# Kernel optimization log

Measured on AMD Instinct MI355X. Metric: run time of the kernel, lower is better.

Reference implementation:

```python
import jax, jax.numpy as jnp
import numpy as np

B, C, H, W = 16, 512, 32, 32
KC = C // 8  # key_channels = 64


def setup_inputs() -> dict:
    key = jax.random.key(0)
    ks = jax.random.split(key, 6)
    s_in = 1.0 / np.sqrt(C)
    return {
        "x": jax.random.normal(ks[0], (B, C, H, W), dtype=jnp.float32),
        "Wq": jax.random.normal(ks[1], (KC, C), dtype=jnp.float32) * s_in,
        "bq": jnp.zeros((KC,), dtype=jnp.float32),
        "Wk": jax.random.normal(ks[2], (KC, C), dtype=jnp.float32) * s_in,
        "bk": jnp.zeros((KC,), dtype=jnp.float32),
        "Wv": jax.random.normal(ks[3], (C, C), dtype=jnp.float32) * s_in,
        "bv": jnp.zeros((C,), dtype=jnp.float32),
        "Wo": jax.random.normal(ks[4], (C, C), dtype=jnp.float32) * s_in,
        "bo": jnp.zeros((C,), dtype=jnp.float32),
        "gamma": jnp.zeros((1,), dtype=jnp.float32),
    }


def reference(x, Wq, bq, Wk, bk, Wv, bv, Wo, bo, gamma):
    b, c, h, w = x.shape
    n = h * w
    kc = Wq.shape[0]
    xf = x.reshape(b, c, n)  # [B, C, N]
    # 1x1 convs == channel matmuls
    q = jnp.einsum('kc,bcn->bnk', Wq, xf) + bq  # [B, N, KC]
    k = jnp.einsum('kc,bcn->bkn', Wk, xf) + bk[None, :, None]  # [B, KC, N]
    v = jnp.einsum('vc,bcn->bnv', Wv, xf) + bv  # [B, N, C]
    scale = jnp.asarray(kc, x.dtype) ** -0.5
    att = jax.nn.softmax(jnp.einsum('bnk,bkm->bnm', q, k) * scale, axis=-1)  # [B, N, N]
    out = jnp.einsum('bnm,bmv->bnv', att, v)  # [B, N, C]
    out = jnp.einsum('cv,bnv->bcn', Wo, out) + bo[None, :, None]  # [B, C, N]
    out = gamma[0] * out + xf
    return out.reshape(b, c, h, w)
```

## Files before the change

### kernel.cpp

```cpp
#include <hip/hip_runtime.h>
#include <cstddef>


typedef unsigned short ushort_t;
typedef __attribute__((ext_vector_type(8))) short bf16x8;
typedef __attribute__((ext_vector_type(4))) float f32x4;
typedef __attribute__((ext_vector_type(2))) float f32x2;
typedef __attribute__((ext_vector_type(2))) unsigned u32x2;

#define QSCALE 0.18033688011112042f

__device__ __forceinline__ ushort_t f2bf_t(float f) {
  return (ushort_t)(__float_as_uint(f) >> 16);
}
__device__ __forceinline__ unsigned pk2bf(float lo, float hi) {
  return __builtin_amdgcn_perm(__float_as_uint(hi), __float_as_uint(lo),
                               0x07060302u);
}

__device__ __forceinline__ void gload16(const ushort_t* g, ushort_t* l) {
  __builtin_amdgcn_global_load_lds(
      (const __attribute__((address_space(1))) void*)g,
      (__attribute__((address_space(3))) void*)l, 16, 0, 0);
}

template <int TM>
__device__ __forceinline__ void gemm_core(
    const ushort_t* __restrict__ A, int lda,
    const ushort_t* __restrict__ B, int ldb,
    int K, int m0, int n0,
    ushort_t* As, ushort_t* Bs, f32x4 (*acc)[4])
{
  constexpr int MT  = TM / 32;
  constexpr int WTM = TM / 2;
  const int t = threadIdx.x;
  const int lane = t & 63, quad = lane >> 4, l15 = lane & 15;
  const int w = t >> 6, wm = w >> 1, wn = w & 1;
  const int rr = (lane >> 3) & 7;
  const int gg = (lane & 7) ^ rr;

  auto stage = [&](int k0, int pbuf) {
    ushort_t* Ad = As + pbuf * (TM * 64);
    ushort_t* Bd = Bs + pbuf * (128 * 64);
    #pragma unroll
    for (int i = 0; i < TM / 32; ++i) {
      const int mrow = w * (TM / 4) + i * 8;
      gload16(A + (size_t)(m0 + mrow + rr) * lda + k0 + gg * 8, Ad + mrow * 64);
    }
    #pragma unroll
    for (int i = 0; i < 4; ++i) {
      const int mrow = w * 32 + i * 8;
      gload16(B + (size_t)(n0 + mrow + rr) * ldb + k0 + gg * 8, Bd + mrow * 64);
    }
  };

  stage(0, 0);

  #pragma unroll
  for (int i = 0; i < MT; ++i)
    #pragma unroll
    for (int j = 0; j < 4; ++j) acc[i][j] = (f32x4){0.f, 0.f, 0.f, 0.f};

  __syncthreads();

  int pb = 0;
  for (int k0 = 0; k0 < K; k0 += 64) {
    if (k0 + 64 < K) stage(k0 + 64, pb ^ 1);
    const ushort_t* Ac = As + pb * (TM * 64);
    const ushort_t* Bc = Bs + pb * (128 * 64);
    #pragma unroll
    for (int kk = 0; kk < 2; ++kk) {
      const int gq = kk * 4 + quad;
      const int sg = (gq ^ (l15 & 7)) * 8;
      bf16x8 af[MT], bfr[4];
      #pragma unroll
      for (int i = 0; i < MT; ++i)
        af[i] = *(const bf16x8*)(Ac + (wm * WTM + i * 16 + l15) * 64 + sg);
      #pragma unroll
      for (int j = 0; j < 4; ++j)
        bfr[j] = *(const bf16x8*)(Bc + (wn * 64 + j * 16 + l15) * 64 + sg);
      #pragma unroll
      for (int i = 0; i < MT; ++i)
        #pragma unroll
        for (int j = 0; j < 4; ++j)
          acc[i][j] = __builtin_amdgcn_mfma_f32_16x16x32_bf16(
              af[i], bfr[j], acc[i][j], 0, 0, 0);
    }
    __syncthreads();
    pb ^= 1;
  }
}

template <int TM, class F>
__device__ __forceinline__ void store_bf16(
    ushort_t* lds, ushort_t* __restrict__ out, int ldo, int m0, int n0,
    f32x4 (*acc)[4], F f)
{
  constexpr int MT = TM / 32, WTM = TM / 2, SI = TM / 16;
  const int t = threadIdx.x;
  const int lane = t & 63, quad = lane >> 4, l15 = lane & 15;
  const int w = t >> 6, wm = w >> 1, wn = w & 1;
  #pragma unroll
  for (int i = 0; i < MT; ++i)
    #pragma unroll
    for (int j = 0; j < 4; ++j)
      #pragma unroll
      for (int r = 0; r < 4; ++r) {
        const int rl = wm * WTM + i * 16 + quad * 4 + r;
        const int cl = wn * 64 + j * 16 + l15;
        lds[rl * 136 + cl] = f2bf_t(f(i, j, r, rl, cl, acc[i][j][r]));
      }
  __syncthreads();
  #pragma unroll
  for (int i = 0; i < SI; ++i) {
    const int s = i * 256 + t, m = s >> 4, g = s & 15;
    const uint4 v = *(const uint4*)(lds + m * 136 + g * 8);
    *(uint4*)(out + (size_t)(m0 + m) * ldo + n0 + g * 8) = v;
  }
}

__global__ __launch_bounds__(256) void prep_x(
    const float* __restrict__ x,
    const float* __restrict__ Wq, const float* __restrict__ Wk,
    const float* __restrict__ Wv, const float* __restrict__ Wo,
    ushort_t* __restrict__ xbfT, ushort_t* __restrict__ Wqk,
    ushort_t* __restrict__ Wvb, ushort_t* __restrict__ Wob)
{
  __shared__ float T[64 * 66];
  const int t = threadIdx.x;
  if (blockIdx.y == 8) {
    const int id = blockIdx.z * 16 + blockIdx.x;
    #pragma unroll
    for (int p = 0; p < 5; ++p) {
      const int s = p * 256 + t;
      if (s < 1152) {
        const int u = id * 1152 + s;
        const int e = u * 2;
        float f0, f1;
        if (e < 32768)       { f0 = Wq[e];         f1 = Wq[e + 1]; }
        else if (e < 65536)  { f0 = Wk[e - 32768]; f1 = Wk[e - 32767]; }
        else if (e < 327680) { f0 = Wv[e - 65536]; f1 = Wv[e - 65535]; }
        else                 { f0 = Wo[e - 327680]; f1 = Wo[e - 327679]; }
        const unsigned pk = pk2bf(f0, f1);
        if (e < 65536)       *((unsigned*)Wqk + u) = pk;
        else if (e < 327680) *((unsigned*)Wvb + (u - 32768)) = pk;
        else                 *((unsigned*)Wob + (u - 163840)) = pk;
      }
    }
    return;
  }
  const int b = blockIdx.z, c0 = blockIdx.y * 64, n0 = blockIdx.x * 64;
  const float* xb = x + ((size_t)b * 512 + c0) * 1024 + n0;
  const int njf = t & 15, ci0 = t >> 4;
  #pragma unroll
  for (int p = 0; p < 4; ++p) {
    const int ci = p * 16 + ci0;
    const f32x4 v = *(const f32x4*)(xb + (size_t)ci * 1024 + njf * 4);
    float* d = &T[ci * 66 + njf * 4];
    *(f32x2*)(d)     = (f32x2){v[0], v[1]};
    *(f32x2*)(d + 2) = (f32x2){v[2], v[3]};
  }
  __syncthreads();
  const int c4 = (t & 15) * 4, nr0 = t >> 4;
  #pragma unroll
  for (int p = 0; p < 4; ++p) {
    const int nr = p * 16 + nr0;
    const float a0 = T[(c4 + 0) * 66 + nr];
    const float a1 = T[(c4 + 1) * 66 + nr];
    const float a2 = T[(c4 + 2) * 66 + nr];
    const float a3 = T[(c4 + 3) * 66 + nr];
    const u32x2 pkv = {pk2bf(a0, a1), pk2bf(a2, a3)};
    *(u32x2*)&xbfT[((size_t)b * 1024 + n0 + nr) * 512 + c0 + c4] = pkv;
  }
}

__global__ __launch_bounds__(256) void k1_fused(
    const ushort_t* __restrict__ xbfT, const ushort_t* __restrict__ Wqk,
    const ushort_t* __restrict__ Wvb,
    const float* __restrict__ bq, const float* __restrict__ bk,
    const float* __restrict__ bv,
    ushort_t* __restrict__ qkt, ushort_t* __restrict__ vt2)
{
  __shared__ __align__(16) ushort_t lds[32768];
  const unsigned lin = blockIdx.x;
  const unsigned wid = (lin & 7) * 96 + (lin >> 3);
  const int b = wid / 48, r = wid % 48;
  const int t = threadIdx.x, lane = t & 63, quad = lane >> 4, l15 = lane & 15;
  const int w = t >> 6, wm = w >> 1, wn = w & 1;
  if (r < 32) {
    const int m0 = (r >> 3) * 128, n0 = (r & 7) * 128;
    f32x4 acc[4][4];
    gemm_core<128>(Wvb, 512, xbfT + (size_t)b * 524288, 512, 512, m0, n0,
                   lds, lds + 16384, acc);
    float br[4][4];
    #pragma unroll
    for (int i = 0; i < 4; ++i)
      #pragma unroll
      for (int rr2 = 0; rr2 < 4; ++rr2)
        br[i][rr2] = bv[m0 + wm * 64 + i * 16 + quad * 4 + rr2];
    store_bf16<128>(lds, vt2 + (size_t)b * 524288, 1024, m0, n0, acc,
        [&](int i, int, int rr2, int, int, float v) { return v + br[i][rr2]; });
  } else {
    const int m0 = (r - 32) * 64;
    f32x4 acc[2][4];
    gemm_core<64>(xbfT + (size_t)b * 524288, 512, Wqk, 512, 512, m0, 0,
                  lds, lds + 8192, acc);
    float bc[4], qs[4];
    #pragma unroll
    for (int j = 0; j < 4; ++j) {
      const int col = wn * 64 + j * 16 + l15;
      bc[j] = (col < 64) ? bq[col] : bk[col - 64];
      qs[j] = (col < 64) ? QSCALE : 1.0f;
    }
    store_bf16<64>(lds, qkt + (size_t)b * 131072, 128, m0, 0, acc,
        [&](int, int j, int, int, int, float v) { return (v + bc[j]) * qs[j]; });
  }
}

__global__ __launch_bounds__(256) void flash_attn(
    const ushort_t* __restrict__ qkt, const ushort_t* __restrict__ vt2,
    ushort_t* __restrict__ o1)
{
  __shared__ __align__(16) ushort_t buf[33792];
  __shared__ float lsum[64][2];
  ushort_t* Ks0 = buf;
  ushort_t* Vs0 = buf + 8192;
  ushort_t* Ps0 = buf + 24576;

  const int t = threadIdx.x;
  const int lane = t & 63, quad = lane >> 4, l15 = lane & 15;
  const int w = t >> 6, wm = w >> 1, wn = w & 1;
  const int rr = (lane >> 3) & 7, gg = (lane & 7) ^ rr;

  const unsigned lin = blockIdx.x;
  const unsigned wid = (lin & 7) * 128 + (lin >> 3);
  const int b  = wid >> 6;
  const int m0 = ((wid >> 2) & 15) * 64;
  const int c0 = (wid & 3) * 128;

  const ushort_t* qb = qkt + (size_t)b * 131072;
  const ushort_t* vb = vt2 + (size_t)b * 524288;

  #pragma unroll
  for (int i = 0; i < 2; ++i) {
    const int mrow = w * 16 + i * 8;
    gload16(qb + (size_t)(m0 + mrow + rr) * 128 + gg * 8, Ps0 + mrow * 64);
  }
  asm volatile("s_waitcnt vmcnt(0)" ::: "memory");
  __builtin_amdgcn_s_barrier();

  bf16x8 af_q[2][2];
  #pragma unroll
  for (int kk = 0; kk < 2; ++kk) {
    const int sg = ((kk * 4 + quad) ^ (l15 & 7)) * 8;
    #pragma unroll
    for (int i = 0; i < 2; ++i)
      af_q[i][kk] = *(const bf16x8*)(Ps0 + (wm * 32 + i * 16 + l15) * 64 + sg);
  }

  const ushort_t* kp = qb + (size_t)(w * 16 + rr) * 128 + 64 + gg * 8;
  const ushort_t* vp = vb + (size_t)(c0 + w * 32 + rr) * 1024 + gg * 8;

  #pragma unroll
  for (int i = 0; i < 2; ++i)
    gload16(kp + i * 1024, Ks0 + (w * 16 + i * 8) * 64);
  #pragma unroll
  for (int i = 0; i < 4; ++i)
    gload16(vp + i * 8192, Vs0 + (w * 32 + i * 8) * 64);
  asm volatile("s_waitcnt vmcnt(0) lgkmcnt(0)" ::: "memory");
  __builtin_amdgcn_s_barrier();

  f32x4 accO[2][4];
  #pragma unroll
  for (int i = 0; i < 2; ++i)
    #pragma unroll
    for (int j = 0; j < 4; ++j) accO[i][j] = (f32x4){0.f, 0.f, 0.f, 0.f};
  float rsum[2][4] = {{0.f, 0.f, 0.f, 0.f}, {0.f, 0.f, 0.f, 0.f}};

  const int psw_off = (wm * 32 + quad * 4) * 72 + wn * 32 + l15;
  const int sg0 = (quad ^ (l15 & 7)) * 8;
  const int sg1 = ((4 + quad) ^ (l15 & 7)) * 8;

  const ushort_t* kpn = kp + 8192;
  const ushort_t* vpn = vp + 64;
  int p = 0;

  #pragma unroll 1
  for (int mc = 0; mc < 1024; mc += 64) {
    ushort_t* Ksd = p ? Ks0 + 4096 : Ks0;
    ushort_t* Vsd = p ? Vs0 + 8192 : Vs0;
    ushort_t* Psd = p ? Ps0 + 4608 : Ps0;
    ushort_t* Ksn = p ? Ks0 : Ks0 + 4096;
    ushort_t* Vsn = p ? Vs0 : Vs0 + 8192;

    if (mc < 960) {
      #pragma unroll
      for (int i = 0; i < 2; ++i)
        gload16(kpn + i * 1024, Ksn + (w * 16 + i * 8) * 64);
      #pragma unroll
      for (int i = 0; i < 4; ++i)
        gload16(vpn + i * 8192, Vsn + (w * 32 + i * 8) * 64);
    }

    f32x4 accS[2][2];
    #pragma unroll
    for (int i = 0; i < 2; ++i)
      #pragma unroll
      for (int j = 0; j < 2; ++j) accS[i][j] = (f32x4){0.f, 0.f, 0.f, 0.f};
    #pragma unroll
    for (int kk = 0; kk < 2; ++kk) {
      const int sg = kk ? sg1 : sg0;
      bf16x8 bk_[2];
      #pragma unroll
      for (int j = 0; j < 2; ++j)
        bk_[j] = *(const bf16x8*)(Ksd + (wn * 32 + j * 16 + l15) * 64 + sg);
      #pragma unroll
      for (int i = 0; i < 2; ++i)
        #pragma unroll
        for (int j = 0; j < 2; ++j)
          accS[i][j] = __builtin_amdgcn_mfma_f32_16x16x32_bf16(
              af_q[i][kk], bk_[j], accS[i][j], 0, 0, 0);
    }

    ushort_t* psw = Psd + psw_off;
    #pragma unroll
    for (int i = 0; i < 2; ++i)
      #pragma unroll
      for (int j = 0; j < 2; ++j)
        #pragma unroll
        for (int r2 = 0; r2 < 4; ++r2) {
          const float e = __builtin_amdgcn_exp2f(accS[i][j][r2]);
          rsum[i][r2] += e;
          psw[(i * 16 + r2) * 72 + j * 16] = f2bf_t(e);
        }

    asm volatile("s_waitcnt lgkmcnt(0)" ::: "memory");
    __builtin_amdgcn_s_barrier();

    #pragma unroll
    for (int kk = 0; kk < 2; ++kk) {
      const int gq = kk * 4 + quad;
      const int sgv = kk ? sg1 : sg0;
      bf16x8 ap[2], bv_[4];
      #pragma unroll
      for (int i = 0; i < 2; ++i)
        ap[i] = *(const bf16x8*)(Psd + (wm * 32 + i * 16 + l15) * 72 + gq * 8);
      #pragma unroll
      for (int j = 0; j < 4; ++j)
        bv_[j] = *(const bf16x8*)(Vsd + (wn * 64 + j * 16 + l15) * 64 + sgv);
      #pragma unroll
      for (int i = 0; i < 2; ++i)
        #pragma unroll
        for (int j = 0; j < 4; ++j)
          accO[i][j] = __builtin_amdgcn_mfma_f32_16x16x32_bf16(
              ap[i], bv_[j], accO[i][j], 0, 0, 0);
    }

    asm volatile("s_waitcnt vmcnt(0)" ::: "memory");
    __builtin_amdgcn_s_barrier();

    kpn += 8192;
    vpn += 64;
    p ^= 1;
  }

  #pragma unroll
  for (int i = 0; i < 2; ++i)
    #pragma unroll
    for (int r2 = 0; r2 < 4; ++r2) {
      float s = rsum[i][r2];
      #pragma unroll
      for (int d = 1; d < 16; d <<= 1) s += __shfl_xor(s, d, 16);
      if (l15 == 0) lsum[wm * 32 + i * 16 + quad * 4 + r2][wn] = s;
    }
  __syncthreads();

  ushort_t* fl_b = buf;
  #pragma unroll
  for (int i = 0; i < 2; ++i)
    #pragma unroll
    for (int r2 = 0; r2 < 4; ++r2) {
      const int row = wm * 32 + i * 16 + quad * 4 + r2;
      const float inv = 1.0f / (lsum[row][0] + lsum[row][1]);
      #pragma unroll
      for (int j = 0; j < 4; ++j)
        fl_b[row * 136 + wn * 64 + j * 16 + l15] = f2bf_t(accO[i][j][r2] * inv);
    }
  __syncthreads();
  #pragma unroll
  for (int pp = 0; pp < 4; ++pp) {
    const int s = pp * 256 + t, m = s >> 4, g = s & 15;
    const uint4 v = *(const uint4*)(fl_b + m * 136 + g * 8);
    *(uint4*)(o1 + ((size_t)b * 1024 + m0 + m) * 512 + c0 + g * 8) = v;
  }
}

__global__ __launch_bounds__(256) void k4_proj(
    const ushort_t* __restrict__ Wob, const ushort_t* __restrict__ o1,
    const float* __restrict__ bo, const float* __restrict__ gamma,
    const float* __restrict__ x, float* __restrict__ out)
{
  __shared__ __align__(16) ushort_t lds[32768];
  const unsigned lin = blockIdx.x;
  const unsigned wid = (lin & 7) * 64 + (lin >> 3);
  const int b = wid >> 5, rem = wid & 31;
  const int m0 = (rem >> 3) * 128, n0 = (rem & 7) * 128;
  f32x4 acc[4][4];
  gemm_core<128>(Wob, 512, o1 + (size_t)b * 524288, 512, 512, m0, n0,
                 lds, lds + 16384, acc);
  const int t = threadIdx.x, lane = t & 63, quad = lane >> 4, l15 = lane & 15;
  const int w = t >> 6, wm = w >> 1, wn = w & 1;
  const float g = gamma[0];
  float br[4][4];
  #pragma unroll
  for (int i = 0; i < 4; ++i)
    #pragma unroll
    for (int r2 = 0; r2 < 4; ++r2)
      br[i][r2] = bo[m0 + wm * 64 + i * 16 + quad * 4 + r2];
  float* fl = (float*)lds;
  #pragma unroll
  for (int h = 0; h < 2; ++h) {
    if (wm == h) {
      #pragma unroll
      for (int i = 0; i < 4; ++i)
        #pragma unroll
        for (int j = 0; j < 4; ++j)
          #pragma unroll
          for (int r2 = 0; r2 < 4; ++r2)
            fl[(i * 16 + quad * 4 + r2) * 132 + wn * 64 + j * 16 + l15] =
                g * (acc[i][j][r2] + br[i][r2]);
    }
    __syncthreads();
    #pragma unroll
    for (int i2 = 0; i2 < 8; ++i2) {
      const int s = i2 * 256 + t, m = s >> 5, c4 = s & 31;
      f32x4 v = *(const f32x4*)(fl + m * 132 + c4 * 4);
      const size_t gi = ((size_t)b * 512 + m0 + h * 64 + m) * 1024 + n0 + c4 * 4;
      const f32x4 xr = *(const f32x4*)(x + gi);
      v += xr;
      *(f32x4*)(out + gi) = v;
    }
    __syncthreads();
  }
}

extern "C" void kernel_launch(void* const* d_in, const int* in_sizes, int n_in,
                              void* d_out, int out_size, void* d_ws, size_t ws_size,
                              hipStream_t stream) {
  const float* x     = (const float*)d_in[0];
  const float* Wq    = (const float*)d_in[1];
  const float* bq    = (const float*)d_in[2];
  const float* Wk    = (const float*)d_in[3];
  const float* bk    = (const float*)d_in[4];
  const float* Wv    = (const float*)d_in[5];
  const float* bv    = (const float*)d_in[6];
  const float* Wo    = (const float*)d_in[7];
  const float* bo    = (const float*)d_in[8];
  const float* gamma = (const float*)d_in[9];
  float* out = (float*)d_out;

  char* wsp = (char*)d_ws;
  ushort_t* xbfT   = (ushort_t*)wsp;  wsp += (size_t)16 * 1024 * 512 * 2;
  ushort_t* Wqk_bf = (ushort_t*)wsp;  wsp += (size_t)128 * 512 * 2;
  ushort_t* Wv_bf  = (ushort_t*)wsp;  wsp += (size_t)512 * 512 * 2;
  ushort_t* Wo_bf  = (ushort_t*)wsp;  wsp += (size_t)512 * 512 * 2;
  ushort_t* qkt    = (ushort_t*)wsp;  wsp += (size_t)16 * 1024 * 128 * 2;
  ushort_t* vt2    = (ushort_t*)wsp;  wsp += (size_t)16 * 512 * 1024 * 2;
  ushort_t* o1     = xbfT;

  prep_x    <<<dim3(16, 9, 16), 256, 0, stream>>>(x, Wq, Wk, Wv, Wo,
                                                  xbfT, Wqk_bf, Wv_bf, Wo_bf);
  k1_fused  <<<768, 256, 0, stream>>>(xbfT, Wqk_bf, Wv_bf, bq, bk, bv, qkt, vt2);
  flash_attn<<<dim3(1024), 256, 0, stream>>>(qkt, vt2, o1);
  k4_proj   <<<512, 256, 0, stream>>>(Wo_bf, o1, bo, gamma, x, out);
}
```

Before: 179.0 us.

## Use 512-thread blocks with 8 waves and drop double buffering in GEMM and attention

Moves the GEMM, attention and projection kernels to 512-thread blocks of 8 waves. Each wave now computes a smaller sub-tile, and the QK GEMM tile grows to 128 rows, so fewer blocks are launched. Double-buffered LDS prefetch with hand-placed waitcnt/barrier is replaced by single-buffered load-sync-compute loops, which cuts LDS use per block. The cost is load latency no longer overlapping compute and more barriers per iteration, traded for more waves per block to hide latency.

```diff
diff --git a/kernel.cpp b/kernel.cpp
--- a/kernel.cpp
+++ b/kernel.cpp
@@ -24,96 +24,75 @@
       (__attribute__((address_space(3))) void*)l, 16, 0, 0);
 }
 
-template <int TM>
-__device__ __forceinline__ void gemm_core(
+__device__ __forceinline__ void gemm512(
     const ushort_t* __restrict__ A, int lda,
     const ushort_t* __restrict__ B, int ldb,
-    int K, int m0, int n0,
-    ushort_t* As, ushort_t* Bs, f32x4 (*acc)[4])
-{
-  constexpr int MT  = TM / 32;
-  constexpr int WTM = TM / 2;
+    int m0, int n0, ushort_t* As, ushort_t* Bs, f32x4 (*acc)[2])
+{
   const int t = threadIdx.x;
   const int lane = t & 63, quad = lane >> 4, l15 = lane & 15;
-  const int w = t >> 6, wm = w >> 1, wn = w & 1;
+  const int w = t >> 6, wm = w >> 2, wn4 = w & 3;
   const int rr = (lane >> 3) & 7;
   const int gg = (lane & 7) ^ rr;
 
-  auto stage = [&](int k0, int pbuf) {
-    ushort_t* Ad = As + pbuf * (TM * 64);
-    ushort_t* Bd = Bs + pbuf * (128 * 64);
-    #pragma unroll
-    for (int i = 0; i < TM / 32; ++i) {
-      const int mrow = w * (TM / 4) + i * 8;
-      gload16(A + (size_t)(m0 + mrow + rr) * lda + k0 + gg * 8, Ad + mrow * 64);
-    }
-    #pragma unroll
-    for (int i = 0; i < 4; ++i) {
-      const int mrow = w * 32 + i * 8;
-      gload16(B + (size_t)(n0 + mrow + rr) * ldb + k0 + gg * 8, Bd + mrow * 64);
-    }
-  };
-
-  stage(0, 0);
-
-  #pragma unroll
-  for (int i = 0; i < MT; ++i)
-    #pragma unroll
-    for (int j = 0; j < 4; ++j) acc[i][j] = (f32x4){0.f, 0.f, 0.f, 0.f};
-
-  __syncthreads();
-
-  int pb = 0;
-  for (int k0 = 0; k0 < K; k0 += 64) {
-    if (k0 + 64 < K) stage(k0 + 64, pb ^ 1);
-    const ushort_t* Ac = As + pb * (TM * 64);
-    const ushort_t* Bc = Bs + pb * (128 * 64);
+  #pragma unroll
+  for (int i = 0; i < 4; ++i)
+    #pragma unroll
+    for (int j = 0; j < 2; ++j) acc[i][j] = (f32x4){0.f, 0.f, 0.f, 0.f};
+
+  for (int k0 = 0; k0 < 512; k0 += 64) {
+    __syncthreads();
+    #pragma unroll
+    for (int i = 0; i < 2; ++i) {
+      const int mrow = w * 16 + i * 8;
+      gload16(A + (size_t)(m0 + mrow + rr) * lda + k0 + gg * 8, As + mrow * 64);
+      gload16(B + (size_t)(n0 + mrow + rr) * ldb + k0 + gg * 8, Bs + mrow * 64);
+    }
+    __syncthreads();
     #pragma unroll
     for (int kk = 0; kk < 2; ++kk) {
       const int gq = kk * 4 + quad;
       const int sg = (gq ^ (l15 & 7)) * 8;
-      bf16x8 af[MT], bfr[4];
-      #pragma unroll
-      for (int i = 0; i < MT; ++i)
-        af[i] = *(const bf16x8*)(Ac + (wm * WTM + i * 16 + l15) * 64 + sg);
-      #pragma unroll
-      for (int j = 0; j < 4; ++j)
-        bfr[j] = *(const bf16x8*)(Bc + (wn * 64 + j * 16 + l15) * 64 + sg);
-      #pragma unroll
-      for (int i = 0; i < MT; ++i)
+      bf16x8 af[4], bfr[2];
+      #pragma unroll
+      for (int i = 0; i < 4; ++i)
+        af[i] = *(const bf16x8*)(As + (wm * 64 + i * 16 + l15) * 64 + sg);
+      #pragma unroll
+      for (int j = 0; j < 2; ++j)
+        bfr[j] = *(const bf16x8*)(Bs + (wn4 * 32 + j * 16 + l15) * 64 + sg);
+      #pragma unroll
+      for (int i = 0; i < 4; ++i)
         #pragma unroll
-        for (int j = 0; j < 4; ++j)
+        for (int j = 0; j < 2; ++j)
           acc[i][j] = __builtin_amdgcn_mfma_f32_16x16x32_bf16(
               af[i], bfr[j], acc[i][j], 0, 0, 0);
     }
-    __syncthreads();
-    pb ^= 1;
-  }
-}
-
-template <int TM, class F>
-__device__ __forceinline__ void store_bf16(
+  }
+  __syncthreads();
+}
+
+template <class F>
+__device__ __forceinline__ void store_bf16_512(
     ushort_t* lds, ushort_t* __restrict__ out, int ldo, int m0, int n0,
-    f32x4 (*acc)[4], F f)
-{
-  constexpr int MT = TM / 32, WTM = TM / 2, SI = TM / 16;
+    f32x4 (*acc)[2], F f)
+{
   const int t = threadIdx.x;
   const int lane = t & 63, quad = lane >> 4, l15 = lane & 15;
-  const int w = t >> 6, wm = w >> 1, wn = w & 1;
-  #pragma unroll
-  for (int i = 0; i < MT; ++i)
-    #pragma unroll
-    for (int j = 0; j < 4; ++j)
+  const int w = t >> 6, wm = w >> 2, wn4 = w & 3;
+  #pragma unroll
+  for (int i = 0; i < 4; ++i)
+    #pragma unroll
+    for (int j = 0; j < 2; ++j)
       #pragma unroll
       for (int r = 0; r < 4; ++r) {
-        const int rl = wm * WTM + i * 16 + quad * 4 + r;
-        const int cl = wn * 64 + j * 16 + l15;
-        lds[rl * 136 + cl] = f2bf_t(f(i, j, r, rl, cl, acc[i][j][r]));
+        const int rl = wm * 64 + i * 16 + quad * 4 + r;
+        const int cl = wn4 * 32 + j * 16 + l15;
+        lds[rl * 136 + cl] = f2bf_t(f(i, j, r, acc[i][j][r]));
       }
   __syncthreads();
   #pragma unroll
-  for (int i = 0; i < SI; ++i) {
-    const int s = i * 256 + t, m = s >> 4, g = s & 15;
+  for (int i = 0; i < 4; ++i) {
+    const int s = i * 512 + t, m = s >> 4, g = s & 15;
     const uint4 v = *(const uint4*)(lds + m * 136 + g * 8);
     *(uint4*)(out + (size_t)(m0 + m) * ldo + n0 + g * 8) = v;
   }
@@ -174,101 +153,82 @@
   }
 }
 
-__global__ __launch_bounds__(256) void k1_fused(
+__global__ __launch_bounds__(512) void k1_fused(
     const ushort_t* __restrict__ xbfT, const ushort_t* __restrict__ Wqk,
     const ushort_t* __restrict__ Wvb,
     const float* __restrict__ bq, const float* __restrict__ bk,
     const float* __restrict__ bv,
     ushort_t* __restrict__ qkt, ushort_t* __restrict__ vt2)
 {
-  __shared__ __align__(16) ushort_t lds[32768];
+  __shared__ __align__(16) ushort_t lds[17408];
   const unsigned lin = blockIdx.x;
-  const unsigned wid = (lin & 7) * 96 + (lin >> 3);
-  const int b = wid / 48, r = wid % 48;
+  const unsigned wid = (lin & 7) * 80 + (lin >> 3);
+  const int b = wid / 40, r = wid % 40;
   const int t = threadIdx.x, lane = t & 63, quad = lane >> 4, l15 = lane & 15;
-  const int w = t >> 6, wm = w >> 1, wn = w & 1;
+  const int w = t >> 6, wm = w >> 2, wn4 = w & 3;
+  f32x4 acc[4][2];
   if (r < 32) {
     const int m0 = (r >> 3) * 128, n0 = (r & 7) * 128;
-    f32x4 acc[4][4];
-    gemm_core<128>(Wvb, 512, xbfT + (size_t)b * 524288, 512, 512, m0, n0,
-                   lds, lds + 16384, acc);
+    gemm512(Wvb, 512, xbfT + (size_t)b * 524288, 512, m0, n0,
+            lds, lds + 8192, acc);
     float br[4][4];
     #pragma unroll
     for (int i = 0; i < 4; ++i)
       #pragma unroll
-      for (int rr2 = 0; rr2 < 4; ++rr2)
-        br[i][rr2] = bv[m0 + wm * 64 + i * 16 + quad * 4 + rr2];
-    store_bf16<128>(lds, vt2 + (size_t)b * 524288, 1024, m0, n0, acc,
-        [&](int i, int, int rr2, int, int, float v) { return v + br[i][rr2]; });
+      for (int r2 = 0; r2 < 4; ++r2)
+        br[i][r2] = bv[m0 + wm * 64 + i * 16 + quad * 4 + r2];
+    store_bf16_512(lds, vt2 + (size_t)b * 524288, 1024, m0, n0, acc,
+        [&](int i, int, int r2, float v) { return v + br[i][r2]; });
   } else {
-    const int m0 = (r - 32) * 64;
-    f32x4 acc[2][4];
-    gemm_core<64>(xbfT + (size_t)b * 524288, 512, Wqk, 512, 512, m0, 0,
-                  lds, lds + 8192, acc);
-    float bc[4], qs[4];
-    #pragma unroll
-    for (int j = 0; j < 4; ++j) {
-      const int col = wn * 64 + j * 16 + l15;
+    const int m0 = (r - 32) * 128;
+    gemm512(xbfT + (size_t)b * 524288, 512, Wqk, 512, m0, 0,
+            lds, lds + 8192, acc);
+    float bc[2], qs[2];
+    #pragma unroll
+    for (int j = 0; j < 2; ++j) {
+      const int col = wn4 * 32 + j * 16 + l15;
       bc[j] = (col < 64) ? bq[col] : bk[col - 64];
       qs[j] = (col < 64) ? QSCALE : 1.0f;
     }
-    store_bf16<64>(lds, qkt + (size_t)b * 131072, 128, m0, 0, acc,
-        [&](int, int j, int, int, int, float v) { return (v + bc[j]) * qs[j]; });
-  }
-}
-
-__global__ __launch_bounds__(256) void flash_attn(
+    store_bf16_512(lds, qkt + (size_t)b * 131072, 128, m0, 0, acc,
+        [&](int, int j, int, float v) { return (v + bc[j]) * qs[j]; });
+  }
+}
+
+__global__ __launch_bounds__(512) void flash_attn(
     const ushort_t* __restrict__ qkt, const ushort_t* __restrict__ vt2,
     ushort_t* __restrict__ o1)
 {
-  __shared__ __align__(16) ushort_t buf[33792];
-  __shared__ float lsum[64][2];
-  ushort_t* Ks0 = buf;
-  ushort_t* Vs0 = buf + 8192;
-  ushort_t* Ps0 = buf + 24576;
+  __shared__ __align__(16) ushort_t buf[25088];
+  __shared__ float lsum[64][4];
+  ushort_t* Ks = buf;
+  ushort_t* Vs = buf + 4096;
+  ushort_t* Ps = buf + 20480;
 
   const int t = threadIdx.x;
   const int lane = t & 63, quad = lane >> 4, l15 = lane & 15;
-  const int w = t >> 6, wm = w >> 1, wn = w & 1;
+  const int w = t >> 6, wm = w >> 2, wn4 = w & 3;
   const int rr = (lane >> 3) & 7, gg = (lane & 7) ^ rr;
 
   const unsigned lin = blockIdx.x;
-  const unsigned wid = (lin & 7) * 128 + (lin >> 3);
-  const int b  = wid >> 6;
-  const int m0 = ((wid >> 2) & 15) * 64;
-  const int c0 = (wid & 3) * 128;
+  const unsigned wid = (lin & 7) * 64 + (lin >> 3);
+  const int b  = wid >> 5;
+  const int m0 = ((wid >> 1) & 15) * 64;
+  const int c0 = (wid & 1) * 256;
 
   const ushort_t* qb = qkt + (size_t)b * 131072;
   const ushort_t* vb = vt2 + (size_t)b * 524288;
 
-  #pragma unroll
-  for (int i = 0; i < 2; ++i) {
-    const int mrow = w * 16 + i * 8;
-    gload16(qb + (size_t)(m0 + mrow + rr) * 128 + gg * 8, Ps0 + mrow * 64);
-  }
-  asm volatile("s_waitcnt vmcnt(0)" ::: "memory");
-  __builtin_amdgcn_s_barrier();
-
+  gload16(qb + (size_t)(m0 + w * 8 + rr) * 128 + gg * 8, Ps + (w * 8) * 64);
+  __syncthreads();
   bf16x8 af_q[2][2];
   #pragma unroll
   for (int kk = 0; kk < 2; ++kk) {
     const int sg = ((kk * 4 + quad) ^ (l15 & 7)) * 8;
     #pragma unroll
     for (int i = 0; i < 2; ++i)
-      af_q[i][kk] = *(const bf16x8*)(Ps0 + (wm * 32 + i * 16 + l15) * 64 + sg);
-  }
-
-  const ushort_t* kp = qb + (size_t)(w * 16 + rr) * 128 + 64 + gg * 8;
-  const ushort_t* vp = vb + (size_t)(c0 + w * 32 + rr) * 1024 + gg * 8;
-
-  #pragma unroll
-  for (int i = 0; i < 2; ++i)
-    gload16(kp + i * 1024, Ks0 + (w * 16 + i * 8) * 64);
-  #pragma unroll
-  for (int i = 0; i < 4; ++i)
-    gload16(vp + i * 8192, Vs0 + (w * 32 + i * 8) * 64);
-  asm volatile("s_waitcnt vmcnt(0) lgkmcnt(0)" ::: "memory");
-  __builtin_amdgcn_s_barrier();
+      af_q[i][kk] = *(const bf16x8*)(Ps + (wm * 32 + i * 16 + l15) * 64 + sg);
+  }
 
   f32x4 accO[2][4];
   #pragma unroll
@@ -277,65 +237,42 @@
     for (int j = 0; j < 4; ++j) accO[i][j] = (f32x4){0.f, 0.f, 0.f, 0.f};
   float rsum[2][4] = {{0.f, 0.f, 0.f, 0.f}, {0.f, 0.f, 0.f, 0.f}};
 
-  const int psw_off = (wm * 32 + quad * 4) * 72 + wn * 32 + l15;
+  ushort_t* ps_w = Ps + (wm * 32 + quad * 4) * 72 + wn4 * 16 + l15;
   const int sg0 = (quad ^ (l15 & 7)) * 8;
   const int sg1 = ((4 + quad) ^ (l15 & 7)) * 8;
 
-  const ushort_t* kpn = kp + 8192;
-  const ushort_t* vpn = vp + 64;
-  int p = 0;
-
   #pragma unroll 1
   for (int mc = 0; mc < 1024; mc += 64) {
-    ushort_t* Ksd = p ? Ks0 + 4096 : Ks0;
-    ushort_t* Vsd = p ? Vs0 + 8192 : Vs0;
-    ushort_t* Psd = p ? Ps0 + 4608 : Ps0;
-    ushort_t* Ksn = p ? Ks0 : Ks0 + 4096;
-    ushort_t* Vsn = p ? Vs0 : Vs0 + 8192;
-
-    if (mc < 960) {
-      #pragma unroll
-      for (int i = 0; i < 2; ++i)
-        gload16(kpn + i * 1024, Ksn + (w * 16 + i * 8) * 64);
-      #pragma unroll
-      for (int i = 0; i < 4; ++i)
-        gload16(vpn + i * 8192, Vsn + (w * 32 + i * 8) * 64);
-    }
-
-    f32x4 accS[2][2];
-    #pragma unroll
-    for (int i = 0; i < 2; ++i)
-      #pragma unroll
-      for (int j = 0; j < 2; ++j) accS[i][j] = (f32x4){0.f, 0.f, 0.f, 0.f};
+    __syncthreads();
+    gload16(qb + (size_t)(mc + w * 8 + rr) * 128 + 64 + gg * 8,
+            Ks + (w * 8) * 64);
+    #pragma unroll
+    for (int i = 0; i < 4; ++i)
+      gload16(vb + (size_t)(c0 + w * 32 + i * 8 + rr) * 1024 + mc + gg * 8,
+              Vs + (w * 32 + i * 8) * 64);
+    __syncthreads();
+
+    f32x4 accS[2];
+    accS[0] = (f32x4){0.f, 0.f, 0.f, 0.f};
+    accS[1] = (f32x4){0.f, 0.f, 0.f, 0.f};
     #pragma unroll
     for (int kk = 0; kk < 2; ++kk) {
       const int sg = kk ? sg1 : sg0;
-      bf16x8 bk_[2];
-      #pragma unroll
-      for (int j = 0; j < 2; ++j)
-        bk_[j] = *(const bf16x8*)(Ksd + (wn * 32 + j * 16 + l15) * 64 + sg);
+      const bf16x8 bk_ = *(const bf16x8*)(Ks + (wn4 * 16 + l15) * 64 + sg);
       #pragma unroll
       for (int i = 0; i < 2; ++i)
-        #pragma unroll
-        for (int j = 0; j < 2; ++j)
-          accS[i][j] = __builtin_amdgcn_mfma_f32_16x16x32_bf16(
-              af_q[i][kk], bk_[j], accS[i][j], 0, 0, 0);
-    }
-
-    ushort_t* psw = Psd + psw_off;
+        accS[i] = __builtin_amdgcn_mfma_f32_16x16x32_bf16(
+            af_q[i][kk], bk_, accS[i], 0, 0, 0);
+    }
     #pragma unroll
     for (int i = 0; i < 2; ++i)
       #pragma unroll
-      for (int j = 0; j < 2; ++j)
-        #pragma unroll
-        for (int r2 = 0; r2 < 4; ++r2) {
-          const float e = __builtin_amdgcn_exp2f(accS[i][j][r2]);
-          rsum[i][r2] += e;
-          psw[(i * 16 + r2) * 72 + j * 16] = f2bf_t(e);
-        }
-
-    asm volatile("s_waitcnt lgkmcnt(0)" ::: "memory");
-    __builtin_amdgcn_s_barrier();
+      for (int r2 = 0; r2 < 4; ++r2) {
+        const float e = __builtin_amdgcn_exp2f(accS[i][r2]);
+        rsum[i][r2] += e;
+        ps_w[(i * 16 + r2) * 72] = f2bf_t(e);
+      }
+    __syncthreads();
 
     #pragma unroll
     for (int kk = 0; kk < 2; ++kk) {
@@ -344,10 +281,10 @@
       bf16x8 ap[2], bv_[4];
       #pragma unroll
       for (int i = 0; i < 2; ++i)
-        ap[i] = *(const bf16x8*)(Psd + (wm * 32 + i * 16 + l15) * 72 + gq * 8);
+        ap[i] = *(const bf16x8*)(Ps + (wm * 32 + i * 16 + l15) * 72 + gq * 8);
       #pragma unroll
       for (int j = 0; j < 4; ++j)
-        bv_[j] = *(const bf16x8*)(Vsd + (wn * 64 + j * 16 + l15) * 64 + sgv);
+        bv_[j] = *(const bf16x8*)(Vs + (wn4 * 64 + j * 16 + l15) * 64 + sgv);
       #pragma unroll
       for (int i = 0; i < 2; ++i)
         #pragma unroll
@@ -355,13 +292,6 @@
           accO[i][j] = __builtin_amdgcn_mfma_f32_16x16x32_bf16(
               ap[i], bv_[j], accO[i][j], 0, 0, 0);
     }
-
-    asm volatile("s_waitcnt vmcnt(0)" ::: "memory");
-    __builtin_amdgcn_s_barrier();
-
-    kpn += 8192;
-    vpn += 64;
-    p ^= 1;
   }
 
   #pragma unroll
@@ -371,7 +301,7 @@
       float s = rsum[i][r2];
       #pragma unroll
       for (int d = 1; d < 16; d <<= 1) s += __shfl_xor(s, d, 16);
-      if (l15 == 0) lsum[wm * 32 + i * 16 + quad * 4 + r2][wn] = s;
+      if (l15 == 0) lsum[wm * 32 + i * 16 + quad * 4 + r2][wn4] = s;
     }
   __syncthreads();
 
@@ -381,35 +311,36 @@
     #pragma unroll
     for (int r2 = 0; r2 < 4; ++r2) {
       const int row = wm * 32 + i * 16 + quad * 4 + r2;
-      const float inv = 1.0f / (lsum[row][0] + lsum[row][1]);
+      const float inv = 1.0f / (lsum[row][0] + lsum[row][1] +
+                                lsum[row][2] + lsum[row][3]);
       #pragma unroll
       for (int j = 0; j < 4; ++j)
-        fl_b[row * 136 + wn * 64 + j * 16 + l15] = f2bf_t(accO[i][j][r2] * inv);
-    }
-  __syncthreads();
-  #pragma unroll
-  for (int pp = 0; pp < 4; ++pp) {
-    const int s = pp * 256 + t, m = s >> 4, g = s & 15;
-    const uint4 v = *(const uint4*)(fl_b + m * 136 + g * 8);
+        fl_b[row * 264 + wn4 * 64 + j * 16 + l15] = f2bf_t(accO[i][j][r2] * inv);
+    }
+  __syncthreads();
+  #pragma unroll
+  for (int pp = 0; pp < 2; ++pp) {
+    const int s = pp * 512 + t, m = s >> 4, g = s & 15;
+    const uint4 v = *(const uint4*)(fl_b + m * 264 + g * 8);
     *(uint4*)(o1 + ((size_t)b * 1024 + m0 + m) * 512 + c0 + g * 8) = v;
   }
 }
 
-__global__ __launch_bounds__(256) void k4_proj(
+__global__ __launch_bounds__(512) void k4_proj(
     const ushort_t* __restrict__ Wob, const ushort_t* __restrict__ o1,
     const float* __restrict__ bo, const float* __restrict__ gamma,
     const float* __restrict__ x, float* __restrict__ out)
 {
-  __shared__ __align__(16) ushort_t lds[32768];
+  __shared__ __align__(16) ushort_t lds[17408];
   const unsigned lin = blockIdx.x;
   const unsigned wid = (lin & 7) * 64 + (lin >> 3);
   const int b = wid >> 5, rem = wid & 31;
   const int m0 = (rem >> 3) * 128, n0 = (rem & 7) * 128;
-  f32x4 acc[4][4];
-  gemm_core<128>(Wob, 512, o1 + (size_t)b * 524288, 512, 512, m0, n0,
-                 lds, lds + 16384, acc);
+  f32x4 acc[4][2];
+  gemm512(Wob, 512, o1 + (size_t)b * 524288, 512, m0, n0,
+          lds, lds + 8192, acc);
   const int t = threadIdx.x, lane = t & 63, quad = lane >> 4, l15 = lane & 15;
-  const int w = t >> 6, wm = w >> 1, wn = w & 1;
+  const int w = t >> 6, wm = w >> 2, wn4 = w & 3;
   const float g = gamma[0];
   float br[4][4];
   #pragma unroll
@@ -424,16 +355,16 @@
       #pragma unroll
       for (int i = 0; i < 4; ++i)
         #pragma unroll
-        for (int j = 0; j < 4; ++j)
+        for (int j = 0; j < 2; ++j)
           #pragma unroll
           for (int r2 = 0; r2 < 4; ++r2)
-            fl[(i * 16 + quad * 4 + r2) * 132 + wn * 64 + j * 16 + l15] =
+            fl[(i * 16 + quad * 4 + r2) * 132 + wn4 * 32 + j * 16 + l15] =
                 g * (acc[i][j][r2] + br[i][r2]);
     }
     __syncthreads();
     #pragma unroll
-    for (int i2 = 0; i2 < 8; ++i2) {
-      const int s = i2 * 256 + t, m = s >> 5, c4 = s & 31;
+    for (int i2 = 0; i2 < 4; ++i2) {
+      const int s = i2 * 512 + t, m = s >> 5, c4 = s & 31;
       f32x4 v = *(const f32x4*)(fl + m * 132 + c4 * 4);
       const size_t gi = ((size_t)b * 512 + m0 + h * 64 + m) * 1024 + n0 + c4 * 4;
       const f32x4 xr = *(const f32x4*)(x + gi);
@@ -470,7 +401,7 @@
 
   prep_x    <<<dim3(16, 9, 16), 256, 0, stream>>>(x, Wq, Wk, Wv, Wo,
                                                   xbfT, Wqk_bf, Wv_bf, Wo_bf);
-  k1_fused  <<<768, 256, 0, stream>>>(xbfT, Wqk_bf, Wv_bf, bq, bk, bv, qkt, vt2);
-  flash_attn<<<dim3(1024), 256, 0, stream>>>(qkt, vt2, o1);
-  k4_proj   <<<512, 256, 0, stream>>>(Wo_bf, o1, bo, gamma, x, out);
-}
+  k1_fused  <<<640, 512, 0, stream>>>(xbfT, Wqk_bf, Wv_bf, bq, bk, bv, qkt, vt2);
+  flash_attn<<<512, 512, 0, stream>>>(qkt, vt2, o1);
+  k4_proj   <<<512, 512, 0, stream>>>(Wo_bf, o1, bo, gamma, x, out);
+}
```

After: 162.4 us. 1.1x faster.
